# Kernel tuning notes

Hardware: AMD Instinct MI355X
Metric: run time of the kernel (lower is better)

The kernel has to match this reference:

```python
import jax, jax.numpy as jnp
import numpy as np

B, N, C = 64, 8192, 64
C4 = C // 4
EPS_BN = 1e-5


def setup_inputs() -> dict:
    key = jax.random.key(0)
    ks = jax.random.split(key, 12)
    s = 0.05
    return {
        "x": jax.random.normal(ks[0], (B, N, 10), jnp.float32),
        "y": jax.random.normal(ks[1], (B, N, 13), jnp.float32),
        "W_l": jax.random.normal(ks[2], (10, C), jnp.float32) * s,
        "b_l": jax.random.normal(ks[3], (C,), jnp.float32) * s,
        "W_r": jax.random.normal(ks[4], (13, C), jnp.float32) * s,
        "b_r": jax.random.normal(ks[5], (C,), jnp.float32) * s,
        "W_qk": jax.random.normal(ks[6], (C4, C), jnp.float32) * s,  # shared q/k 1x1-conv weight
        "W_v": jax.random.normal(ks[7], (C, C), jnp.float32) * s,
        "b_v": jax.random.normal(ks[8], (C,), jnp.float32) * s,
        "W_t": jax.random.normal(ks[9], (C, C), jnp.float32) * s,
        "b_t": jax.random.normal(ks[10], (C,), jnp.float32) * s,
        "gamma": jnp.ones((C,), jnp.float32),
        "beta": jnp.zeros((C,), jnp.float32),
    }


def reference(x, y, W_l, b_l, W_r, b_r, W_qk, W_v, b_v, W_t, b_t, gamma, beta):
    # x: [B,N,10] -> linear_l; y: [B,N,13] -> linear_r  (torch keeps [B,C,N]; we keep [B,N,C])
    X = x @ W_l + b_l                                   # [B,N,C]
    Y = y @ W_r + b_r                                   # [B,N,C]
    # 1x1 convs == per-point matmuls; attention runs ACROSS the batch dim per point n
    xq = jnp.einsum('bnc,dc->nbd', X, W_qk)             # [N,B,C/4]
    yk = jnp.einsum('bnc,dc->nbd', Y, W_qk)             # [N,B,C/4] (shared weight)
    yv = jnp.einsum('bnc,dc->nbd', Y, W_v) + b_v        # [N,B,C]
    energy = jnp.einsum('nbd,ned->nbe', xq, yk)         # [N,B,B]
    attn = jax.nn.softmax(energy, axis=-1)
    # extra L1 renormalization over dim=1 (offset-attention style)
    attn = attn / (1e-9 + attn.sum(axis=1, keepdims=True))
    yr = jnp.einsum('nbe,nec->bnc', attn, yv)           # [B,N,C]
    # trans_conv -> BatchNorm (training-mode batch stats) -> ReLU -> residual -> max over points
    t = jnp.einsum('bnc,dc->bnd', X - yr, W_t) + b_t    # [B,N,C]
    mean = t.mean(axis=(0, 1))
    var = t.var(axis=(0, 1))                            # biased var, as BN uses
    tn = gamma * (t - mean) * jax.lax.rsqrt(var + EPS_BN) + beta
    xres = X + jax.nn.relu(tn)                          # [B,N,C]
    return jnp.max(xres, axis=1)[:, :, None]            # [B,C,1] to match torch layout
```

## Files before the change

### kernel.cpp

```cpp
#include <hip/hip_runtime.h>

#define B_ 64
#define N_ 8192

using short8 = __attribute__((ext_vector_type(8))) short;
using f32x4  = __attribute__((ext_vector_type(4))) float;

#define MFMA16(a, b, c) __builtin_amdgcn_mfma_f32_16x16x32_bf16((a), (b), (c), 0, 0, 0)

__device__ inline unsigned short f2bf(float f) {
  union { float f; unsigned int u; } v; v.f = f;
  return (unsigned short)((v.u + 0x8000u) >> 16);
}
__device__ inline float bf2f(unsigned int hi16_in_low) {
  union { unsigned int u; float f; } v; v.u = hi16_in_low << 16;
  return v.f;
}
__device__ inline unsigned u2(float a, float b) {
  return (unsigned)f2bf(a) | ((unsigned)f2bf(b) << 16);
}
__device__ inline void put_y(short* Ar0, short* YT0, int b, int f, unsigned short h) {
  const int s = (f >= 13) ? 1 : 0;
  Ar0[16 + f + 2547 * s] = (short)h;
  YT0[f * 72 + b + 216 * s] = (short)h;
}


__global__ void k0_prep(const float* __restrict__ W_l, const float* __restrict__ b_l,
                        const float* __restrict__ W_r, const float* __restrict__ b_r,
                        const float* __restrict__ W_qk, const float* __restrict__ W_v,
                        const float* __restrict__ b_v, const float* __restrict__ W_t,
                        float* __restrict__ wsf) {
  const int tid = threadIdx.x;
  unsigned short* wb   = (unsigned short*)(wsf + 66688);
  unsigned short* BM   = wb;
  unsigned short* BL   = wb + 512;
  unsigned short* BRV2 = wb + 2560;
  unsigned short* BT   = wb + 4608;
  if (blockIdx.x == 0) {
    __shared__ float Wlq[11 * 16], Wrk[14 * 16];
    for (int idx = tid; idx < 11 * 16; idx += 256) {
      int i = idx >> 4, d = idx & 15;
      const float* a = (i < 10) ? (W_l + i * 64) : b_l;
      float s = 0.f;
      for (int c = 0; c < 64; ++c) s = fmaf(a[c], W_qk[d * 64 + c], s);
      Wlq[idx] = s;
    }
    for (int idx = tid; idx < 14 * 16; idx += 256) {
      int j = idx >> 4, d = idx & 15;
      const float* a = (j < 13) ? (W_r + j * 64) : b_r;
      float s = 0.f;
      for (int c = 0; c < 64; ++c) s = fmaf(a[c], W_qk[d * 64 + c], s);
      Wrk[idx] = s;
    }
    __syncthreads();
    for (int idx = tid; idx < 512; idx += 256) {
      int j = idx >> 5, kk = idx & 31;
      unsigned short o = 0;
      if (j < 14 && kk < 11) {
        float s = 0.f;
        for (int d = 0; d < 16; ++d) s = fmaf(Wlq[kk * 16 + d], Wrk[j * 16 + d], s);
        o = f2bf(s);
      }
      BM[idx] = o;
    }
  } else if (blockIdx.x == 1) {
    for (int idx = tid; idx < 2048; idx += 256) {
      int c = idx >> 5, kk = idx & 31;
      unsigned short o = 0;
      if (kk < 13) {
        float s = 0.f;
        for (int j = 0; j < 64; ++j) s = fmaf(W_r[kk * 64 + j], W_v[c * 64 + j], s);
        o = f2bf(s);
      } else if (kk == 13) {
        float s = b_v[c];
        for (int j = 0; j < 64; ++j) s = fmaf(b_r[j], W_v[c * 64 + j], s);
        o = f2bf(s);
      }
      BRV2[idx] = o;
    }
  } else if (blockIdx.x == 2) {
    for (int idx = tid; idx < 2048; idx += 256) {
      int c = idx >> 5, kk = idx & 31;
      unsigned short o = 0;
      if (kk < 10) o = f2bf(W_l[kk * 64 + c]);
      else if (kk == 10) o = f2bf(b_l[c]);
      BL[idx] = o;
    }
    for (int i = tid; i < 1024; i += 256) wsf[i] = 0.f;
  } else {
    for (int i = tid; i < 4096; i += 256) BT[i] = f2bf(W_t[i]);
  }
}

__global__ __launch_bounds__(256, 4)
void k1_attn(const float* __restrict__ x, const float* __restrict__ y,
             const float* __restrict__ wsf, const float* __restrict__ b_t,
             float* __restrict__ stats) {
  __shared__ __align__(16) short lds[18688];
  float* const scr = (float*)lds;
  short* const Axy[2] = {lds, lds + 2560};
  short* const YTb[2] = {lds + 5120, lds + 6272};
  short* const awB    = lds + 7424;
  short* const guB    = lds + 16640;

  const unsigned short* wb   = (const unsigned short*)(wsf + 66688);
  const unsigned short* BM   = wb;
  const unsigned short* BL   = wb + 512;
  const unsigned short* BRV2 = wb + 2560;
  const unsigned short* BT   = wb + 4608;
  unsigned short* tg = (unsigned short*)(wsf + 66688) + 8704;

  const int tid  = threadIdx.x;
  const int w    = tid >> 6;
  const int lane = tid & 63;
  const int l15  = lane & 15;
  const int q    = lane >> 4;
  const int r0   = w * 16;
  const int n0   = blockIdx.x * 2;
  short* const aw[2] = {awB + w * 1152, awB + (4 + w) * 1152};
  short* const gu[2] = {guB + w * 256,  guB + (4 + w) * 256};

  {
    const int b = tid >> 2, i = tid & 3;
    const float* xb = x + ((size_t)b * N_ + n0) * 10;
    const float* yb = y + ((size_t)b * N_ + n0) * 13;
    short* const Ar0 = Axy[0] + b * 40;
    short* const Ar1 = Axy[1] + b * 40;
    short* const YT0 = YTb[0];
    {
      const float4 v = *(const float4*)(xb + 4 * i);
      const int g0 = 4 * i, g1 = 4 * i + 2;
      *(unsigned*)(Ar0 + (g0 >= 10 ? g0 + 2550 : g0)) = u2(v.x, v.y);
      *(unsigned*)(Ar0 + (g1 >= 10 ? g1 + 2550 : g1)) = u2(v.z, v.w);
      if (i == 0) {
        const float4 vv = *(const float4*)(xb + 16);
        *(unsigned*)(Ar1 + 6) = u2(vv.x, vv.y);
        *(unsigned*)(Ar1 + 8) = u2(vv.z, vv.w);
      }
    }
    if (i == 1) { *(unsigned*)(Ar1 + 10) = 0x3F80u; *(unsigned*)(Ar1 + 12) = 0u; *(unsigned*)(Ar1 + 14) = 0u; }
    if (i == 2) { *(unsigned*)(Ar0 + 10) = 0x3F80u; *(unsigned*)(Ar0 + 12) = 0u; *(unsigned*)(Ar0 + 14) = 0u; }
#pragma unroll
    for (int t = 0; t < 3; ++t) {
      const int j = i + 4 * t;
      const float2 v = *(const float2*)(yb + 2 * j);
      put_y(Ar0, YT0, b, 2 * j,     f2bf(v.x));
      put_y(Ar0, YT0, b, 2 * j + 1, f2bf(v.y));
    }
    if (i == 0) {
      const float2 v = *(const float2*)(yb + 24);
      put_y(Ar0, YT0, b, 24, f2bf(v.x));
      put_y(Ar0, YT0, b, 25, f2bf(v.y));
    }
    if (i == 3) {
      Ar0[29] = (short)0x3F80; *(unsigned*)(Ar0 + 30) = 0u;
      YT0[13 * 72 + b] = (short)0x3F80; YT0[14 * 72 + b] = 0; YT0[15 * 72 + b] = 0;
    }
    if (i == 2) {
      Ar1[29] = (short)0x3F80; *(unsigned*)(Ar1 + 30) = 0u;
      short* YT1 = YT0 + 1152;
      YT1[13 * 72 + b] = (short)0x3F80; YT1[14 * 72 + b] = 0; YT1[15 * 72 + b] = 0;
    }
  }
  asm volatile("s_waitcnt lgkmcnt(0)" ::: "memory");
  __builtin_amdgcn_sched_barrier(0);

  const short8 z8 = {0, 0, 0, 0, 0, 0, 0, 0};
  const f32x4 zero4 = {0.f, 0.f, 0.f, 0.f};

  const short8 bmF = *(const short8*)&BM[l15 * 32 + q * 8];
  short8 blF[4];
#pragma unroll
  for (int f = 0; f < 4; ++f) blF[f] = *(const short8*)&BL[(f * 16 + l15) * 32 + q * 8];

  f32x4 X[2][4];
  __builtin_amdgcn_s_setprio(1);
#pragma unroll
  for (int p = 0; p < 2; ++p) {
    const short8 aA = *(const short8*)&Axy[p][(r0 + l15) * 40 + q * 8];
    f32x4 G = MFMA16(aA, bmF, zero4);
#pragma unroll
    for (int f = 0; f < 4; ++f) X[p][f] = MFMA16(aA, blF[f], zero4);
#pragma unroll
    for (int j = 0; j < 4; ++j) gu[p][(q * 4 + j) * 16 + l15] = (short)f2bf(G[j]);
  }
  __builtin_amdgcn_s_setprio(0);
  __syncthreads();

  f32x4 E[2][4];
  __builtin_amdgcn_s_setprio(1);
#pragma unroll
  for (int p = 0; p < 2; ++p) {
    short8 aG = z8;
    if (q < 2) aG = *(const short8*)&gu[p][l15 * 16 + q * 8];
#pragma unroll
    for (int f = 0; f < 4; ++f) {
      short8 bk = z8;
      if (q < 2) bk = *(const short8*)&Axy[p][(f * 16 + l15) * 40 + 16 + q * 8];
      E[p][f] = MFMA16(aG, bk, zero4);
    }
  }
  __builtin_amdgcn_s_setprio(0);
  __syncthreads();

  float inv_r[2][4];
#pragma unroll
  for (int p = 0; p < 2; ++p)
#pragma unroll
    for (int j = 0; j < 4; ++j) {
      float s = 0.f;
#pragma unroll
      for (int f = 0; f < 4; ++f) { E[p][f][j] = __expf(E[p][f][j]); s += E[p][f][j]; }
      s += __shfl_xor(s, 1);
      s += __shfl_xor(s, 2);
      s += __shfl_xor(s, 4);
      s += __shfl_xor(s, 8);
      inv_r[p][j] = 1.0f / s;
    }
#pragma unroll
  for (int p = 0; p < 2; ++p)
#pragma unroll
    for (int f = 0; f < 4; ++f) {
      float cs = E[p][f][0] * inv_r[p][0] + E[p][f][1] * inv_r[p][1] +
                 E[p][f][2] * inv_r[p][2] + E[p][f][3] * inv_r[p][3];
      cs += __shfl_xor(cs, 16);
      cs += __shfl_xor(cs, 32);
      if (lane < 16) scr[p * 256 + w * 64 + f * 16 + l15] = cs;
    }
  __syncthreads();

#pragma unroll
  for (int p = 0; p < 2; ++p) {
#pragma unroll
    for (int f = 0; f < 4; ++f) {
      const int col = f * 16 + l15;
      const float* sp = scr + p * 256;
      const float csv = 1.0f / (1e-9f + sp[col] + sp[64 + col] + sp[128 + col] + sp[192 + col]);
#pragma unroll
      for (int j = 0; j < 4; ++j)
        aw[p][(q * 4 + j) * 72 + col] = (short)f2bf(E[p][f][j] * inv_r[p][j] * csv);
    }
  }

  short8 brvF[4];
#pragma unroll
  for (int f = 0; f < 4; ++f) brvF[f] = *(const short8*)&BRV2[(f * 16 + l15) * 32 + q * 8];
  __builtin_amdgcn_s_setprio(1);
#pragma unroll
  for (int p = 0; p < 2; ++p) {
    const short8 aA0 = *(const short8*)&aw[p][l15 * 72 + q * 8];
    const short8 aA1 = *(const short8*)&aw[p][l15 * 72 + 32 + q * 8];
    f32x4 U = MFMA16(aA0, *(const short8*)&YTb[p][l15 * 72 + q * 8], zero4);
    U = MFMA16(aA1, *(const short8*)&YTb[p][l15 * 72 + 32 + q * 8], U);
#pragma unroll
    for (int j = 0; j < 4; ++j) gu[p][(q * 4 + j) * 16 + l15] = (short)f2bf(U[j]);
    short8 aU = z8;
    if (q < 2) aU = *(const short8*)&gu[p][l15 * 16 + q * 8];
#pragma unroll
    for (int f = 0; f < 4; ++f) {
      f32x4 yr = MFMA16(aU, brvF[f], zero4);
#pragma unroll
      for (int j = 0; j < 4; ++j)
        aw[p][(q * 4 + j) * 72 + f * 16 + l15] = (short)f2bf(X[p][f][j] - yr[j]);
    }
  }
  __builtin_amdgcn_s_setprio(0);

  f32x4 t[2][4];
  float sRed[2][4], ssRed[2][4];
  uint2 pk[2][4];
  float4 btv[4];
#pragma unroll
  for (int f = 0; f < 4; ++f) btv[f] = *(const float4*)&b_t[f * 16 + q * 4];
  __builtin_amdgcn_s_setprio(1);
#pragma unroll
  for (int p = 0; p < 2; ++p) {
    const short8 aZ0 = *(const short8*)&aw[p][l15 * 72 + q * 8];
    const short8 aZ1 = *(const short8*)&aw[p][l15 * 72 + 32 + q * 8];
#pragma unroll
    for (int f = 0; f < 4; ++f) {
      const int c = f * 16 + l15;
      const float bT = b_t[c];
      const short8 bt0 = *(const short8*)&BT[c * 64 + q * 8];
      const short8 bt1 = *(const short8*)&BT[c * 64 + 32 + q * 8];
      t[p][f] = MFMA16(aZ0, bt0, ((f32x4){bT, bT, bT, bT}));
      t[p][f] = MFMA16(aZ1, bt1, t[p][f]);
      float s = 0.f, ss = 0.f;
#pragma unroll
      for (int j = 0; j < 4; ++j) { s += t[p][f][j]; ss = fmaf(t[p][f][j], t[p][f][j], ss); }
      s  += __shfl_xor(s, 16);  s  += __shfl_xor(s, 32);
      ss += __shfl_xor(ss, 16); ss += __shfl_xor(ss, 32);
      sRed[p][f] = s; ssRed[p][f] = ss;
      f32x4 tc = MFMA16(bt0, aZ0, ((f32x4){btv[f].x, btv[f].y, btv[f].z, btv[f].w}));
      tc = MFMA16(bt1, aZ1, tc);
      pk[p][f].x = (unsigned)f2bf(tc[0]) | ((unsigned)f2bf(tc[1]) << 16);
      pk[p][f].y = (unsigned)f2bf(tc[2]) | ((unsigned)f2bf(tc[3]) << 16);
    }
  }
  __builtin_amdgcn_s_setprio(0);
  __syncthreads();
#pragma unroll
  for (int p = 0; p < 2; ++p)
#pragma unroll
    for (int f = 0; f < 4; ++f)
      if (lane < 16) {
        scr[p * 512 + w * 64 + f * 16 + l15]       = sRed[p][f];
        scr[p * 512 + 256 + w * 64 + f * 16 + l15] = ssRed[p][f];
      }
  __syncthreads();
  if (tid < 128) {
    const int p = tid >> 6, c = tid & 63;
    const float* sp = scr + p * 512;
    const float s  = sp[c] + sp[64 + c] + sp[128 + c] + sp[192 + c];
    const float ss = sp[256 + c] + sp[320 + c] + sp[384 + c] + sp[448 + c];
    float* st = stats + ((n0 + p) & 7) * 128;
    atomicAdd(&st[c], s);
    atomicAdd(&st[64 + c], ss);
  }
#pragma unroll
  for (int p = 0; p < 2; ++p)
#pragma unroll
    for (int f = 0; f < 4; ++f)
      *(uint2*)&tg[(size_t)(n0 + p) * 4096 + (size_t)(r0 + l15) * 64 + f * 16 + q * 4] =
          pk[p][f];
}

__global__ __launch_bounds__(256)
void k3_max(const float* __restrict__ x, const float* __restrict__ W_l,
            const float* __restrict__ b_l, const float* __restrict__ gamma,
            const float* __restrict__ beta, const unsigned short* __restrict__ tg,
            const float* __restrict__ stats, float* __restrict__ pmax)
{
  const int b = blockIdx.x >> 4;
  const int chunk = blockIdx.x & 15;
  __shared__ __align__(16) float xs[512 * 10];
  __shared__ float mr[128];
  __shared__ float sm[4][64];
  {
    const float4* src = (const float4*)(x + ((size_t)b * N_ + (size_t)chunk * 512) * 10);
    float4* dst = (float4*)xs;
#pragma unroll
    for (int t = 0; t < 5; ++t) dst[threadIdx.x + 256 * t] = src[threadIdx.x + 256 * t];
  }
  if (threadIdx.x < 64) {
    const int c = threadIdx.x;
    float s = 0.f, ss = 0.f;
    for (int r = 0; r < 8; ++r) { s += stats[r * 128 + c]; ss += stats[r * 128 + 64 + c]; }
    const float inv = 1.0f / (float)(B_ * N_);
    const float mu = s * inv;
    const float var = fmaf(ss, inv, -mu * mu);
    mr[c] = mu;
    mr[64 + c] = rsqrtf(var + 1e-5f);
  }
  const int wv = threadIdx.x >> 6;
  const int lane = threadIdx.x & 63;
  const int c0 = (lane & 15) * 4;
  const int nsub = lane >> 4;
  float4 wl4[10];
#pragma unroll
  for (int k = 0; k < 10; ++k) wl4[k] = *(const float4*)&W_l[k * 64 + c0];
  const float4 bl  = *(const float4*)&b_l[c0];
  const float4 g   = *(const float4*)&gamma[c0];
  const float4 be  = *(const float4*)&beta[c0];
  __syncthreads();
  const float4 mu  = *(const float4*)&mr[c0];
  const float4 rs  = *(const float4*)&mr[64 + c0];
  float4 grs, bmb;
  grs.x = g.x * rs.x; grs.y = g.y * rs.y; grs.z = g.z * rs.z; grs.w = g.w * rs.w;
  bmb.x = be.x - mu.x * grs.x; bmb.y = be.y - mu.y * grs.y;
  bmb.z = be.z - mu.z * grs.z; bmb.w = be.w - mu.w * grs.w;
  float4 m = {-1e30f, -1e30f, -1e30f, -1e30f};
  const int ln0 = wv * 128 + nsub;
#pragma unroll 2
  for (int jj = 0; jj < 32; ++jj) {
    const int ln = ln0 + jj * 4;
    const uint2 tv = *(const uint2*)&tg[(size_t)(chunk * 512 + ln) * 4096 + (b << 6) + c0];
    const float2* xr = (const float2*)(xs + ln * 10);
    float4 X = bl;
#pragma unroll
    for (int k = 0; k < 5; ++k) {
      const float2 xk = xr[k];
      X.x = fmaf(xk.x, wl4[2 * k].x, X.x); X.y = fmaf(xk.x, wl4[2 * k].y, X.y);
      X.z = fmaf(xk.x, wl4[2 * k].z, X.z); X.w = fmaf(xk.x, wl4[2 * k].w, X.w);
      X.x = fmaf(xk.y, wl4[2 * k + 1].x, X.x); X.y = fmaf(xk.y, wl4[2 * k + 1].y, X.y);
      X.z = fmaf(xk.y, wl4[2 * k + 1].z, X.z); X.w = fmaf(xk.y, wl4[2 * k + 1].w, X.w);
    }
    const float t0 = bf2f(tv.x & 0xFFFFu), t1 = bf2f(tv.x >> 16);
    const float t2 = bf2f(tv.y & 0xFFFFu), t3 = bf2f(tv.y >> 16);
    m.x = fmaxf(m.x, X.x + fmaxf(fmaf(t0, grs.x, bmb.x), 0.f));
    m.y = fmaxf(m.y, X.y + fmaxf(fmaf(t1, grs.y, bmb.y), 0.f));
    m.z = fmaxf(m.z, X.z + fmaxf(fmaf(t2, grs.z, bmb.z), 0.f));
    m.w = fmaxf(m.w, X.w + fmaxf(fmaf(t3, grs.w, bmb.w), 0.f));
  }
  m.x = fmaxf(m.x, __shfl_xor(m.x, 16)); m.y = fmaxf(m.y, __shfl_xor(m.y, 16));
  m.z = fmaxf(m.z, __shfl_xor(m.z, 16)); m.w = fmaxf(m.w, __shfl_xor(m.w, 16));
  m.x = fmaxf(m.x, __shfl_xor(m.x, 32)); m.y = fmaxf(m.y, __shfl_xor(m.y, 32));
  m.z = fmaxf(m.z, __shfl_xor(m.z, 32)); m.w = fmaxf(m.w, __shfl_xor(m.w, 32));
  if (lane < 16) *(float4*)&sm[wv][c0] = m;
  __syncthreads();
  if (threadIdx.x < 64) {
    const float r = fmaxf(fmaxf(sm[0][threadIdx.x], sm[1][threadIdx.x]),
                          fmaxf(sm[2][threadIdx.x], sm[3][threadIdx.x]));
    pmax[(size_t)blockIdx.x * 64 + threadIdx.x] = r;
  }
}

__global__ void k4_final(const float* __restrict__ pmax, float* __restrict__ out) {
  const int b = blockIdx.x, c = threadIdx.x;
  float m = -1e30f;
  for (int ch = 0; ch < 16; ++ch) m = fmaxf(m, pmax[((size_t)b * 16 + ch) * 64 + c]);
  out[b * 64 + c] = m;
}

extern "C" void kernel_launch(void* const* d_in, const int* in_sizes, int n_in,
                              void* d_out, int out_size, void* d_ws, size_t ws_size,
                              hipStream_t stream) {
  const float* x     = (const float*)d_in[0];
  const float* y     = (const float*)d_in[1];
  const float* W_l   = (const float*)d_in[2];
  const float* b_l   = (const float*)d_in[3];
  const float* W_r   = (const float*)d_in[4];
  const float* b_r   = (const float*)d_in[5];
  const float* W_qk  = (const float*)d_in[6];
  const float* W_v   = (const float*)d_in[7];
  const float* b_v   = (const float*)d_in[8];
  const float* W_t   = (const float*)d_in[9];
  const float* b_t   = (const float*)d_in[10];
  const float* gamma = (const float*)d_in[11];
  const float* beta  = (const float*)d_in[12];
  float* out = (float*)d_out;

  float* wsf = (float*)d_ws;
  float* stats = wsf;
  float* pmax  = wsf + 1152;
  const unsigned short* tg = (const unsigned short*)(wsf + 66688) + 8704;

  hipLaunchKernelGGL(k0_prep, dim3(4), dim3(256), 0, stream,
                     W_l, b_l, W_r, b_r, W_qk, W_v, b_v, W_t, wsf);
  hipLaunchKernelGGL(k1_attn, dim3(N_ / 2), dim3(256), 0, stream,
                     x, y, wsf, b_t, stats);
  hipLaunchKernelGGL(k3_max, dim3(1024), dim3(256), 0, stream,
                     x, W_l, b_l, gamma, beta, tg, stats, pmax);
  hipLaunchKernelGGL(k4_final, dim3(64), dim3(64), 0, stream, pmax, out);
}
```

Measured before the change: 202.7 us.

## Drop barriers in attention kernel and software-pipeline tg loads in max kernel

The attention kernel gets a separate LDS region for the column-sum scratch, which lets it remove one __syncthreads after the energy MFMAs. It also hoists the trans-conv weight fragments out of the inner loop, issues the tg global store before the stats reduction, and removes another barrier. The max kernel now prefetches tg values one block of four rows ahead, so global-load latency overlaps with the X recompute. The cost is more LDS per block and higher register pressure, which may lower occupancy.

```diff
diff --git a/kernel.cpp b/kernel.cpp
--- a/kernel.cpp
+++ b/kernel.cpp
@@ -97,12 +97,13 @@
 void k1_attn(const float* __restrict__ x, const float* __restrict__ y,
              const float* __restrict__ wsf, const float* __restrict__ b_t,
              float* __restrict__ stats) {
-  __shared__ __align__(16) short lds[18688];
-  float* const scr = (float*)lds;
+  __shared__ __align__(16) short lds[19712];
+  float* const statsScr = (float*)lds;
   short* const Axy[2] = {lds, lds + 2560};
   short* const YTb[2] = {lds + 5120, lds + 6272};
   short* const awB    = lds + 7424;
   short* const guB    = lds + 16640;
+  float* const csF    = (float*)(lds + 18688);
 
   const unsigned short* wb   = (const unsigned short*)(wsf + 66688);
   const unsigned short* BM   = wb;
@@ -202,7 +203,6 @@
     }
   }
   __builtin_amdgcn_s_setprio(0);
-  __syncthreads();
 
   float inv_r[2][4];
 #pragma unroll
@@ -226,7 +226,7 @@
                  E[p][f][2] * inv_r[p][2] + E[p][f][3] * inv_r[p][3];
       cs += __shfl_xor(cs, 16);
       cs += __shfl_xor(cs, 32);
-      if (lane < 16) scr[p * 256 + w * 64 + f * 16 + l15] = cs;
+      if (lane < 16) csF[p * 256 + w * 64 + f * 16 + l15] = cs;
     }
   __syncthreads();
 
@@ -235,7 +235,7 @@
 #pragma unroll
     for (int f = 0; f < 4; ++f) {
       const int col = f * 16 + l15;
-      const float* sp = scr + p * 256;
+      const float* sp = csF + p * 256;
       const float csv = 1.0f / (1e-9f + sp[col] + sp[64 + col] + sp[128 + col] + sp[192 + col]);
 #pragma unroll
       for (int j = 0; j < 4; ++j)
@@ -267,12 +267,17 @@
   }
   __builtin_amdgcn_s_setprio(0);
 
-  f32x4 t[2][4];
   float sRed[2][4], ssRed[2][4];
   uint2 pk[2][4];
   float4 btv[4];
-#pragma unroll
-  for (int f = 0; f < 4; ++f) btv[f] = *(const float4*)&b_t[f * 16 + q * 4];
+  short8 btF0[4], btF1[4];
+#pragma unroll
+  for (int f = 0; f < 4; ++f) {
+    btv[f] = *(const float4*)&b_t[f * 16 + q * 4];
+    const int c = f * 16 + l15;
+    btF0[f] = *(const short8*)&BT[c * 64 + q * 8];
+    btF1[f] = *(const short8*)&BT[c * 64 + 32 + q * 8];
+  }
   __builtin_amdgcn_s_setprio(1);
 #pragma unroll
   for (int p = 0; p < 2; ++p) {
@@ -282,48 +287,45 @@
     for (int f = 0; f < 4; ++f) {
       const int c = f * 16 + l15;
       const float bT = b_t[c];
-      const short8 bt0 = *(const short8*)&BT[c * 64 + q * 8];
-      const short8 bt1 = *(const short8*)&BT[c * 64 + 32 + q * 8];
-      t[p][f] = MFMA16(aZ0, bt0, ((f32x4){bT, bT, bT, bT}));
-      t[p][f] = MFMA16(aZ1, bt1, t[p][f]);
+      f32x4 t = MFMA16(aZ0, btF0[f], ((f32x4){bT, bT, bT, bT}));
+      t = MFMA16(aZ1, btF1[f], t);
       float s = 0.f, ss = 0.f;
 #pragma unroll
-      for (int j = 0; j < 4; ++j) { s += t[p][f][j]; ss = fmaf(t[p][f][j], t[p][f][j], ss); }
+      for (int j = 0; j < 4; ++j) { s += t[j]; ss = fmaf(t[j], t[j], ss); }
       s  += __shfl_xor(s, 16);  s  += __shfl_xor(s, 32);
       ss += __shfl_xor(ss, 16); ss += __shfl_xor(ss, 32);
       sRed[p][f] = s; ssRed[p][f] = ss;
-      f32x4 tc = MFMA16(bt0, aZ0, ((f32x4){btv[f].x, btv[f].y, btv[f].z, btv[f].w}));
-      tc = MFMA16(bt1, aZ1, tc);
+      f32x4 tc = MFMA16(btF0[f], aZ0, ((f32x4){btv[f].x, btv[f].y, btv[f].z, btv[f].w}));
+      tc = MFMA16(btF1[f], aZ1, tc);
       pk[p][f].x = (unsigned)f2bf(tc[0]) | ((unsigned)f2bf(tc[1]) << 16);
       pk[p][f].y = (unsigned)f2bf(tc[2]) | ((unsigned)f2bf(tc[3]) << 16);
     }
   }
   __builtin_amdgcn_s_setprio(0);
-  __syncthreads();
+#pragma unroll
+  for (int p = 0; p < 2; ++p)
+#pragma unroll
+    for (int f = 0; f < 4; ++f)
+      *(uint2*)&tg[(size_t)(n0 + p) * 4096 + (size_t)(r0 + l15) * 64 + f * 16 + q * 4] =
+          pk[p][f];
 #pragma unroll
   for (int p = 0; p < 2; ++p)
 #pragma unroll
     for (int f = 0; f < 4; ++f)
       if (lane < 16) {
-        scr[p * 512 + w * 64 + f * 16 + l15]       = sRed[p][f];
-        scr[p * 512 + 256 + w * 64 + f * 16 + l15] = ssRed[p][f];
+        statsScr[p * 512 + w * 64 + f * 16 + l15]       = sRed[p][f];
+        statsScr[p * 512 + 256 + w * 64 + f * 16 + l15] = ssRed[p][f];
       }
   __syncthreads();
   if (tid < 128) {
     const int p = tid >> 6, c = tid & 63;
-    const float* sp = scr + p * 512;
+    const float* sp = statsScr + p * 512;
     const float s  = sp[c] + sp[64 + c] + sp[128 + c] + sp[192 + c];
     const float ss = sp[256 + c] + sp[320 + c] + sp[384 + c] + sp[448 + c];
     float* st = stats + ((n0 + p) & 7) * 128;
     atomicAdd(&st[c], s);
     atomicAdd(&st[64 + c], ss);
   }
-#pragma unroll
-  for (int p = 0; p < 2; ++p)
-#pragma unroll
-    for (int f = 0; f < 4; ++f)
-      *(uint2*)&tg[(size_t)(n0 + p) * 4096 + (size_t)(r0 + l15) * 64 + f * 16 + q * 4] =
-          pk[p][f];
 }
 
 __global__ __launch_bounds__(256)
@@ -372,26 +374,40 @@
   bmb.z = be.z - mu.z * grs.z; bmb.w = be.w - mu.w * grs.w;
   float4 m = {-1e30f, -1e30f, -1e30f, -1e30f};
   const int ln0 = wv * 128 + nsub;
-#pragma unroll 2
-  for (int jj = 0; jj < 32; ++jj) {
-    const int ln = ln0 + jj * 4;
-    const uint2 tv = *(const uint2*)&tg[(size_t)(chunk * 512 + ln) * 4096 + (b << 6) + c0];
-    const float2* xr = (const float2*)(xs + ln * 10);
-    float4 X = bl;
-#pragma unroll
-    for (int k = 0; k < 5; ++k) {
-      const float2 xk = xr[k];
-      X.x = fmaf(xk.x, wl4[2 * k].x, X.x); X.y = fmaf(xk.x, wl4[2 * k].y, X.y);
-      X.z = fmaf(xk.x, wl4[2 * k].z, X.z); X.w = fmaf(xk.x, wl4[2 * k].w, X.w);
-      X.x = fmaf(xk.y, wl4[2 * k + 1].x, X.x); X.y = fmaf(xk.y, wl4[2 * k + 1].y, X.y);
-      X.z = fmaf(xk.y, wl4[2 * k + 1].z, X.z); X.w = fmaf(xk.y, wl4[2 * k + 1].w, X.w);
-    }
-    const float t0 = bf2f(tv.x & 0xFFFFu), t1 = bf2f(tv.x >> 16);
-    const float t2 = bf2f(tv.y & 0xFFFFu), t3 = bf2f(tv.y >> 16);
-    m.x = fmaxf(m.x, X.x + fmaxf(fmaf(t0, grs.x, bmb.x), 0.f));
-    m.y = fmaxf(m.y, X.y + fmaxf(fmaf(t1, grs.y, bmb.y), 0.f));
-    m.z = fmaxf(m.z, X.z + fmaxf(fmaf(t2, grs.z, bmb.z), 0.f));
-    m.w = fmaxf(m.w, X.w + fmaxf(fmaf(t3, grs.w, bmb.w), 0.f));
+  const size_t tgbase = (size_t)(chunk * 512) * 4096 + (b << 6) + c0;
+  uint2 tv[4];
+#pragma unroll
+  for (int u = 0; u < 4; ++u)
+    tv[u] = *(const uint2*)&tg[tgbase + (size_t)(ln0 + u * 4) * 4096];
+  for (int blk = 0; blk < 8; ++blk) {
+    uint2 cur[4];
+#pragma unroll
+    for (int u = 0; u < 4; ++u) cur[u] = tv[u];
+    if (blk < 7) {
+#pragma unroll
+      for (int u = 0; u < 4; ++u)
+        tv[u] = *(const uint2*)&tg[tgbase + (size_t)(ln0 + (blk + 1) * 16 + u * 4) * 4096];
+    }
+#pragma unroll
+    for (int u = 0; u < 4; ++u) {
+      const int ln = ln0 + blk * 16 + u * 4;
+      const float2* xr = (const float2*)(xs + ln * 10);
+      float4 X = bl;
+#pragma unroll
+      for (int k = 0; k < 5; ++k) {
+        const float2 xk = xr[k];
+        X.x = fmaf(xk.x, wl4[2 * k].x, X.x); X.y = fmaf(xk.x, wl4[2 * k].y, X.y);
+        X.z = fmaf(xk.x, wl4[2 * k].z, X.z); X.w = fmaf(xk.x, wl4[2 * k].w, X.w);
+        X.x = fmaf(xk.y, wl4[2 * k + 1].x, X.x); X.y = fmaf(xk.y, wl4[2 * k + 1].y, X.y);
+        X.z = fmaf(xk.y, wl4[2 * k + 1].z, X.z); X.w = fmaf(xk.y, wl4[2 * k + 1].w, X.w);
+      }
+      const float t0 = bf2f(cur[u].x & 0xFFFFu), t1 = bf2f(cur[u].x >> 16);
+      const float t2 = bf2f(cur[u].y & 0xFFFFu), t3 = bf2f(cur[u].y >> 16);
+      m.x = fmaxf(m.x, X.x + fmaxf(fmaf(t0, grs.x, bmb.x), 0.f));
+      m.y = fmaxf(m.y, X.y + fmaxf(fmaf(t1, grs.y, bmb.y), 0.f));
+      m.z = fmaxf(m.z, X.z + fmaxf(fmaf(t2, grs.z, bmb.z), 0.f));
+      m.w = fmaxf(m.w, X.w + fmaxf(fmaf(t3, grs.w, bmb.w), 0.f));
+    }
   }
   m.x = fmaxf(m.x, __shfl_xor(m.x, 16)); m.y = fmaxf(m.y, __shfl_xor(m.y, 16));
   m.z = fmaxf(m.z, __shfl_xor(m.z, 16)); m.w = fmaxf(m.w, __shfl_xor(m.w, 16));
```

Result: no change. 203.2 us (+0.3%).
